# Kernel optimization log

Hardware: AMD Instinct MI355X
Metric: run time of the kernel (lower is better)

The kernel has to match this reference:

```python
import jax, jax.numpy as jnp
import numpy as np

# dims
L, H, ENC, DM, DFF, S, P, B = 2, 8, 862, 512, 2048, 512, 96, 32
HD = DM // H  # per-head q/k/v dim (v_dim = d_model, double_v_dim=False)


def setup_inputs() -> dict:
    key = jax.random.key(0)
    ks = jax.random.split(key, 16)
    rn = lambda k, shape, scale: jax.random.normal(k, shape, jnp.float32) * scale
    return {
        "X": rn(ks[0], (B, S, ENC), 1.0),
        "batch_x_mark": rn(ks[1], (B, S, 4), 1.0),
        "dec_inp": rn(ks[2], (B, P, ENC), 1.0),
        "batch_y_mark": rn(ks[3], (B, P, 4), 1.0),
        # retention params (stacked over layers / heads), init ~ randn/fan_in as in source
        "wq": rn(ks[4], (L, H, ENC, HD), 1.0 / ENC),
        "wk": rn(ks[5], (L, H, ENC, HD), 1.0 / ENC),
        "wv": rn(ks[6], (L, H, ENC, HD), 1.0 / ENC),
        "wg": rn(ks[7], (L, ENC, DM), 1.0 / ENC),
        "wo_ret": rn(ks[8], (L, DM, ENC), 1.0 / ENC),
        "gn_w": jnp.ones((L, DM)), "gn_b": jnp.zeros((L, DM)),
        "ln1_w": jnp.ones((L, ENC)), "ln1_b": jnp.zeros((L, ENC)),
        "ln2_w": jnp.ones((L, ENC)), "ln2_b": jnp.zeros((L, ENC)),
        # SGLU params, init randn/hidden_size as in source
        "sglu_u": rn(ks[9], (L, ENC, DM), 1.0 / DM),
        "sglu_v": rn(ks[10], (L, ENC, DM), 1.0 / DM),
        "sglu_o": rn(ks[11], (L, DM, ENC), 1.0 / DM),
        # temporal projection MLP (Linear init scale)
        "tp_w1": rn(ks[12], (S, DFF), (1.0 / S) ** 0.5),
        "tp_b1": jnp.zeros((DFF,)),
        "tp_w2": rn(ks[13], (DFF, P), (1.0 / DFF) ** 0.5),
        "tp_b2": jnp.zeros((P,)),
    }


def _layernorm(x, w, b, eps=1e-5):
    m = x.mean(-1, keepdims=True)
    v = x.var(-1, keepdims=True)  # biased variance, matches torch LayerNorm
    return (x - m) * jax.lax.rsqrt(v + eps) * w + b


def _decay_mask(seq_len, n_heads):
    # RetNet per-head decays: gamma_h = 1 - exp(linspace(log 1/32, log 1/512, H))
    g = 1.0 - jnp.exp(jnp.linspace(jnp.log(1.0 / 32.0), jnp.log(1.0 / 512.0), n_heads))
    i = jnp.arange(seq_len)
    d = i[:, None] - i[None, :]
    return jnp.where(d >= 0, g[:, None, None] ** jnp.maximum(d, 0), 0.0)  # [H,S,S]


def _retention(x, wq, wk, wv, wg, wo, gnw, gnb, D):
    # x: [B,S,ENC]; wq/wk/wv: [H,ENC,HD]
    Q = jnp.einsum('bsi,hid->bhsd', x, wq)
    K = jnp.einsum('bsi,hid->bhsd', x, wk)
    V = jnp.einsum('bsi,hid->bhsd', x, wv)
    scores = jnp.einsum('bhsd,bhtd->bhst', Q, K) * D  # decay-masked retention
    Y = jnp.einsum('bhst,bhtv->bhsv', scores, V)      # [B,H,S,HD]
    # GroupNorm(groups=H) over concatenated head channels == per-head normalize
    m = Y.mean(-1, keepdims=True)
    v = Y.var(-1, keepdims=True)
    Yn = (Y - m) * jax.lax.rsqrt(v + 1e-5)
    Yn = Yn.transpose(0, 2, 1, 3).reshape(x.shape[0], x.shape[1], -1)  # [B,S,DM]
    Yn = Yn * gnw + gnb
    G = x @ wg
    return (G * jax.nn.sigmoid(G) * Yn) @ wo  # swish gate, project back to ENC


def reference(X, batch_x_mark, dec_inp, batch_y_mark, wq, wk, wv, wg, wo_ret,
              gn_w, gn_b, ln1_w, ln1_b, ln2_w, ln2_b, sglu_u, sglu_v, sglu_o,
              tp_w1, tp_b1, tp_w2, tp_b2):
    D = _decay_mask(X.shape[1], H)
    for i in range(L):
        Y = _retention(_layernorm(X, ln1_w[i], ln1_b[i]), wq[i], wk[i], wv[i],
                       wg[i], wo_ret[i], gn_w[i], gn_b[i], D) + X
        Z = _layernorm(Y, ln2_w[i], ln2_b[i])
        X = ((Z @ sglu_v[i]) * (Z @ sglu_u[i])) @ sglu_o[i] + Y  # SGLU + residual
    T = X.transpose(0, 2, 1)  # [B,ENC,S]
    T = jax.nn.gelu(T @ tp_w1 + tp_b1, approximate=False)
    T = T @ tp_w2 + tp_b2
    return T.transpose(0, 2, 1)  # [B,P,ENC]
```

## Files before the change

kernel.cpp:

```cpp
#include <hip/hip_runtime.h>
#include <cstddef>
#include <cstdint>

#define L_    2
#define H_    8
#define ENC_  862
#define DM_   512
#define DFF_  2048
#define S_    512
#define P_    96
#define B_    32
#define HD_   64
#define EPAD_ 896
#define KPE_  896
#define XLD_  864
#define M1_   (B_*S_)
#define M2_   (B_*EPAD_)

typedef unsigned short u16;
typedef unsigned int   u32;
typedef u16   u16x8 __attribute__((ext_vector_type(8)));
typedef short s16x8 __attribute__((ext_vector_type(8)));
typedef float f32x4 __attribute__((ext_vector_type(4)));

__device__ __forceinline__ float b2f(u16 v) { return __uint_as_float(((u32)v) << 16); }
__device__ __forceinline__ u16 f2b(float f) {
    u32 u = __float_as_uint(f);
    u = (u + 0x7FFF + ((u >> 16) & 1)) >> 16;
    return (u16)u;
}
__device__ __forceinline__ float gelu_exact(float x) {
    return 0.5f * x * (1.f + erff(x * 0.70710678118654752f));
}

typedef __attribute__((address_space(1))) const void gas_void;
typedef __attribute__((address_space(3))) void sas_void;
__device__ __forceinline__ void gload16(const u16* g, u16* l) {
    __builtin_amdgcn_global_load_lds((gas_void*)g, (sas_void*)l, 16, 0, 0);
}

__global__ __launch_bounds__(256) void zgap(u16* __restrict__ p, int n)
{
    int i = blockIdx.x * 256 + threadIdx.x;
    if (i < n) p[i] = 0;
}

template<int MODE, bool RF32>
__global__ __launch_bounds__(256) void mgemm(
    const u16* __restrict__ A, int ldA,
    const u16* __restrict__ BT, int ldBT,
    void* __restrict__ Cv, int ldc,
    const void* __restrict__ R, int ldR,
    int M, int N, int KP)
{
    __shared__ u16 As[128 * 64];
    __shared__ u16 Bs[128 * 64];
    int tid = threadIdx.x;
    int l = tid & 63, w = tid >> 6;
    int m0 = blockIdx.x * 128, n0 = blockIdx.y * 128;
    int wm = (w >> 1) * 64, wn = (w & 1) * 64;
    int fr = l & 15, kb = l >> 4;

    f32x4 acc[4][4];
    #pragma unroll
    for (int i = 0; i < 4; i++)
        #pragma unroll
        for (int j = 0; j < 4; j++)
            acc[i][j] = (f32x4){0.f, 0.f, 0.f, 0.f};

    int arow = tid >> 3, acol = (tid & 7) * 8;
    const u16* ga = A + (size_t)(m0 + arow) * ldA + acol;
    const u16* gb = BT + (size_t)(n0 + arow) * ldBT + acol;
    u16* lA = As + tid * 8;
    u16* lB = Bs + tid * 8;

    for (int kt = 0; kt < KP; kt += 64) {
        #pragma unroll
        for (int c = 0; c < 4; c++) {
            gload16(ga + (size_t)(c * 32) * ldA, lA + c * 2048);
            gload16(gb + (size_t)(c * 32) * ldBT, lB + c * 2048);
        }
        ga += 64; gb += 64;
        __syncthreads();
        #pragma unroll
        for (int ks = 0; ks < 2; ks++) {
            s16x8 af[4], bf[4];
            #pragma unroll
            for (int i = 0; i < 4; i++) {
                af[i] = *(const s16x8*)&As[(wm + i * 16 + fr) * 64 + ks * 32 + kb * 8];
                bf[i] = *(const s16x8*)&Bs[(wn + i * 16 + fr) * 64 + ks * 32 + kb * 8];
            }
            #pragma unroll
            for (int i = 0; i < 4; i++)
                #pragma unroll
                for (int j = 0; j < 4; j++)
                    acc[i][j] = __builtin_amdgcn_mfma_f32_16x16x32_bf16(af[i], bf[j], acc[i][j], 0, 0, 0);
        }
        __syncthreads();
    }

    u16*   Cb = (u16*)Cv;
    float* Cf = (float*)Cv;
    const float* Rf = (const float*)R;
    const u16*   Rb = (const u16*)R;
    #pragma unroll
    for (int i = 0; i < 4; i++) {
        int mrow = m0 + wm + i * 16 + (l >> 4) * 4;
        #pragma unroll
        for (int j = 0; j < 4; j++) {
            int ncol = n0 + wn + j * 16 + (l & 15);
            if (ncol >= N) continue;
            #pragma unroll
            for (int r = 0; r < 4; r++) {
                int m = mrow + r;
                float v = acc[i][j][r];
                if (MODE == 0) {
                    Cb[(size_t)m * ldc + ncol] = f2b(v);
                } else if (MODE == 1) {
                    v += RF32 ? Rf[(size_t)m * ldR + ncol] : b2f(Rb[(size_t)m * ldR + ncol]);
                    Cb[(size_t)m * ldc + ncol] = f2b(v);
                } else if (MODE == 2) {
                    Cb[(size_t)m * ldc + ncol] = f2b(gelu_exact(v + Rf[ncol]));
                } else {
                    int bb = m / EPAD_;
                    int e = m - bb * EPAD_;
                    if (e < ENC_)
                        Cf[((size_t)bb * P_ + ncol) * ENC_ + e] = v + Rf[ncol];
                }
            }
        }
    }
}

template<bool XF32>
__global__ __launch_bounds__(128) void ln_k(const void* __restrict__ xv, int ldin,
                                            const float* __restrict__ w,
                                            const float* __restrict__ b,
                                            u16* __restrict__ y)
{
    int row = blockIdx.x;
    const float* xf = (const float*)xv + (size_t)row * ldin;
    const u16*   xb = (const u16*)xv + (size_t)row * ldin;
    float s = 0.f, q = 0.f;
    for (int c = threadIdx.x; c < ENC_; c += 128) {
        float v = XF32 ? xf[c] : b2f(xb[c]);
        s += v; q += v * v;
    }
    #pragma unroll
    for (int m = 1; m < 64; m <<= 1) { s += __shfl_xor(s, m, 64); q += __shfl_xor(q, m, 64); }
    __shared__ float red[4];
    int wid = threadIdx.x >> 6;
    if ((threadIdx.x & 63) == 0) { red[wid] = s; red[2 + wid] = q; }
    __syncthreads();
    s = red[0] + red[1]; q = red[2] + red[3];
    float mean = s * (1.f / ENC_);
    float var = q * (1.f / ENC_) - mean * mean;
    float rs = rsqrtf(var + 1e-5f);
    u16* yr = y + (size_t)row * XLD_;
    for (int c = threadIdx.x; c < XLD_; c += 128) {
        u16 o = 0;
        if (c < ENC_) {
            float v = XF32 ? xf[c] : b2f(xb[c]);
            o = f2b((v - mean) * rs * w[c] + b[c]);
        }
        yr[c] = o;
    }
}

__global__ __launch_bounds__(256) void repackT(const float* __restrict__ src, u16* __restrict__ dst,
                                               int Nsrc, int Ksrc, int KP, int total)
{
    int idx = blockIdx.x * 256 + threadIdx.x;
    if (idx >= total) return;
    int n = idx / KP, k = idx - n * KP;
    dst[idx] = (k < Ksrc && n < Nsrc) ? f2b(src[(size_t)k * Nsrc + n]) : (u16)0;
}

__global__ __launch_bounds__(256) void repack_qkvg(const float* __restrict__ wq, const float* __restrict__ wk,
                                                   const float* __restrict__ wv, const float* __restrict__ wg,
                                                   u16* __restrict__ dst)
{
    int idx = blockIdx.x * 256 + threadIdx.x;
    if (idx >= 2048 * KPE_) return;
    int n = idx / KPE_, k = idx - n * KPE_;
    u16 v = 0;
    if (k < ENC_) {
        int sec = n >> 9, c = n & 511;
        if (sec == 3) v = f2b(wg[(size_t)k * DM_ + c]);
        else {
            const float* s = (sec == 0) ? wq : (sec == 1) ? wk : wv;
            int h = c >> 6, d = c & 63;
            v = f2b(s[((size_t)h * ENC_ + k) * HD_ + d]);
        }
    }
    dst[idx] = v;
}

__global__ __launch_bounds__(256) void gate1_k(const u16* __restrict__ QKVG,
                                               const u16* __restrict__ Yn,
                                               u16* __restrict__ out)
{
    int i = blockIdx.x * 256 + threadIdx.x;
    int row = i >> 6, col = (i & 63) * 8;
    u16x8 g = *(const u16x8*)&QKVG[(size_t)row * 2048 + 1536 + col];
    u16x8 yv = *(const u16x8*)&Yn[(size_t)row * 512 + col];
    u16x8 o;
    #pragma unroll
    for (int j = 0; j < 8; j++) {
        float gf = b2f(g[j]);
        o[j] = f2b(gf / (1.f + __expf(-gf)) * b2f(yv[j]));
    }
    *(u16x8*)&out[(size_t)row * 512 + col] = o;
}

__global__ __launch_bounds__(256) void gate2_k(const u16* __restrict__ Z, u16* __restrict__ out)
{
    int i = blockIdx.x * 256 + threadIdx.x;
    int row = i >> 6, col = (i & 63) * 8;
    u16x8 a = *(const u16x8*)&Z[(size_t)row * 1024 + col];
    u16x8 b = *(const u16x8*)&Z[(size_t)row * 1024 + 512 + col];
    u16x8 o;
    #pragma unroll
    for (int j = 0; j < 8; j++) o[j] = f2b(b2f(a[j]) * b2f(b[j]));
    *(u16x8*)&out[(size_t)row * 512 + col] = o;
}

__global__ __launch_bounds__(256) void transpose_k(const u16* __restrict__ Xf, u16* __restrict__ XT)
{
    __shared__ u16 t[64][65];
    int b = blockIdx.x, s0 = blockIdx.y * 64, e0 = blockIdx.z * 64;
    int tid = threadIdx.x;
    int sr = tid >> 2, ch = (tid & 3) * 16;
    const u16* src = Xf + ((size_t)(b * S_) + s0 + sr) * ENC_ + e0 + ch;
    #pragma unroll
    for (int i = 0; i < 16; i++)
        t[sr][ch + i] = (e0 + ch + i < ENC_) ? src[i] : (u16)0;
    __syncthreads();
    int er = tid >> 2;
    u16* dst = XT + ((size_t)b * EPAD_ + e0 + er) * 512 + s0 + ch;
    #pragma unroll
    for (int i = 0; i < 16; i++)
        dst[i] = t[ch + i][er];
}

__global__ __launch_bounds__(256) void retention_k(const u16* __restrict__ QKVG,
                                                   const float* __restrict__ gnw,
                                                   const float* __restrict__ gnb,
                                                   u16* __restrict__ Yn)
{
    __shared__ u16 Ks[64 * 72];
    __shared__ u16 Vt[64 * 72];
    __shared__ u16 Pl[64 * 72];
    int tid = threadIdx.x;
    int l = tid & 63, w = tid >> 6;
    int g = l >> 4, fr = l & 15;
    int st = blockIdx.x, bh = blockIdx.y;
    int b = bh >> 3, h = bh & 7;
    int s0 = st * 64;

    const float lo = -3.46573590280f;
    const float hi = -6.23832462504f;
    float gamma = 1.f - expf(lo + (float)h * ((hi - lo) * (1.f / 7.f)));
    float l2g = log2f(gamma);

    size_t qbase = (size_t)(b * S_) * 2048 + h * 64;

    int qs_rel = w * 16 + fr;
    float qscale = exp2f((float)qs_rel * l2g);
    s16x8 qa[2];
    {
        const u16* qsrc = QKVG + qbase + (size_t)(s0 + qs_rel) * 2048;
        #pragma unroll
        for (int ks = 0; ks < 2; ks++) {
            u16x8 raw = *(const u16x8*)(qsrc + ks * 32 + g * 8);
            s16x8 sc;
            #pragma unroll
            for (int e = 0; e < 8; e++) sc[e] = (short)f2b(b2f(raw[e]) * qscale);
            qa[ks] = sc;
        }
    }

    f32x4 accy[4];
    #pragma unroll
    for (int jj = 0; jj < 4; jj++) accy[jj] = (f32x4){0.f, 0.f, 0.f, 0.f};

    int tv = tid >> 2, dv0 = (tid & 3) * 16;

    for (int tt = 0; tt <= st; ++tt) {
        int t0 = tt * 64;
        __syncthreads();
        {
            float kscale = exp2f((float)(s0 - (t0 + tv)) * l2g);
            const u16* ksrc = QKVG + qbase + (size_t)(t0 + tv) * 2048 + 512 + dv0;
            const u16* vsrc = QKVG + qbase + (size_t)(t0 + tv) * 2048 + 1024 + dv0;
            u16x8 k0 = *(const u16x8*)ksrc;
            u16x8 k1 = *(const u16x8*)(ksrc + 8);
            s16x8 o0, o1;
            #pragma unroll
            for (int e = 0; e < 8; e++) {
                o0[e] = (short)f2b(b2f(k0[e]) * kscale);
                o1[e] = (short)f2b(b2f(k1[e]) * kscale);
            }
            *(s16x8*)&Ks[tv * 72 + dv0]     = o0;
            *(s16x8*)&Ks[tv * 72 + dv0 + 8] = o1;
            u16x8 v0 = *(const u16x8*)vsrc;
            u16x8 v1 = *(const u16x8*)(vsrc + 8);
            #pragma unroll
            for (int e = 0; e < 8; e++) {
                Vt[(dv0 + e) * 72 + tv]     = v0[e];
                Vt[(dv0 + 8 + e) * 72 + tv] = v1[e];
            }
        }
        __syncthreads();

        f32x4 ps[4];
        #pragma unroll
        for (int j = 0; j < 4; j++) ps[j] = (f32x4){0.f, 0.f, 0.f, 0.f};
        #pragma unroll
        for (int ks = 0; ks < 2; ks++) {
            #pragma unroll
            for (int j = 0; j < 4; j++) {
                s16x8 kf = *(const s16x8*)&Ks[(j * 16 + fr) * 72 + ks * 32 + g * 8];
                ps[j] = __builtin_amdgcn_mfma_f32_16x16x32_bf16(qa[ks], kf, ps[j], 0, 0, 0);
            }
        }
        bool diag = (tt == st);
        #pragma unroll
        for (int j = 0; j < 4; j++) {
            #pragma unroll
            for (int r = 0; r < 4; r++) {
                int srel = w * 16 + g * 4 + r;
                int tloc = j * 16 + fr;
                float p = ps[j][r];
                if (diag && (srel < tloc)) p = 0.f;
                Pl[srel * 72 + tloc] = f2b(p);
            }
        }
        s16x8 pa0 = *(const s16x8*)&Pl[(w * 16 + fr) * 72 + g * 8];
        s16x8 pa1 = *(const s16x8*)&Pl[(w * 16 + fr) * 72 + 32 + g * 8];
        #pragma unroll
        for (int jj = 0; jj < 4; jj++) {
            s16x8 vb0 = *(const s16x8*)&Vt[(jj * 16 + fr) * 72 + g * 8];
            s16x8 vb1 = *(const s16x8*)&Vt[(jj * 16 + fr) * 72 + 32 + g * 8];
            accy[jj] = __builtin_amdgcn_mfma_f32_16x16x32_bf16(pa0, vb0, accy[jj], 0, 0, 0);
            accy[jj] = __builtin_amdgcn_mfma_f32_16x16x32_bf16(pa1, vb1, accy[jj], 0, 0, 0);
        }
    }

    #pragma unroll
    for (int r = 0; r < 4; r++) {
        float s_ = accy[0][r] + accy[1][r] + accy[2][r] + accy[3][r];
        float q_ = accy[0][r]*accy[0][r] + accy[1][r]*accy[1][r]
                 + accy[2][r]*accy[2][r] + accy[3][r]*accy[3][r];
        #pragma unroll
        for (int m = 1; m < 16; m <<= 1) { s_ += __shfl_xor(s_, m, 64); q_ += __shfl_xor(q_, m, 64); }
        float mean = s_ * (1.f / 64.f);
        float var = q_ * (1.f / 64.f) - mean * mean;
        float rs = rsqrtf(var + 1e-5f);
        int srow = s0 + w * 16 + g * 4 + r;
        #pragma unroll
        for (int jj = 0; jj < 4; jj++) {
            int c0 = h * 64 + jj * 16 + fr;
            Yn[(size_t)(b * S_ + srow) * 512 + c0] =
                f2b((accy[jj][r] - mean) * rs * gnw[c0] + gnb[c0]);
        }
    }
}

extern "C" void kernel_launch(void* const* d_in, const int* in_sizes, int n_in,
                              void* d_out, int out_size, void* d_ws, size_t ws_size,
                              hipStream_t stream)
{
    const float* X    = (const float*)d_in[0];
    const float* wq   = (const float*)d_in[4];
    const float* wk   = (const float*)d_in[5];
    const float* wv   = (const float*)d_in[6];
    const float* wg   = (const float*)d_in[7];
    const float* wo   = (const float*)d_in[8];
    const float* gnw  = (const float*)d_in[9];
    const float* gnb  = (const float*)d_in[10];
    const float* ln1w = (const float*)d_in[11];
    const float* ln1b = (const float*)d_in[12];
    const float* ln2w = (const float*)d_in[13];
    const float* ln2b = (const float*)d_in[14];
    const float* su   = (const float*)d_in[15];
    const float* sv   = (const float*)d_in[16];
    const float* so   = (const float*)d_in[17];
    const float* tw1  = (const float*)d_in[18];
    const float* tb1  = (const float*)d_in[19];
    const float* tw2  = (const float*)d_in[20];
    const float* tb2  = (const float*)d_in[21];
    u16* ws = (u16*)d_ws;

    const size_t NXE = (size_t)M1_ * ENC_;
    const size_t oA  = 0;
    const size_t oB  = (size_t)M1_ * XLD_ + 1024;
    const size_t oC  = oB + (size_t)M1_ * 2048;
    const size_t oD  = oC + (size_t)M1_ * 512;
    const size_t oE  = oD + (size_t)M1_ * 512;
    const size_t oF  = oE + NXE;
    const size_t oW  = oF + NXE;
    const size_t oWqkvg = oW;
    const size_t oWo    = oWqkvg + (size_t)2048 * KPE_;
    const size_t oWsuv  = oWo + (size_t)EPAD_ * 512;
    const size_t oWso   = oWsuv + (size_t)1024 * KPE_;
    const size_t oWt1   = oWso + (size_t)EPAD_ * 512;
    const size_t oWt2   = oWt1 + (size_t)2048 * 512;
    const size_t END    = oWt2 + (size_t)128 * 2048;
    const size_t oXT = 0;
    const size_t oT1 = (size_t)B_ * EPAD_ * 512;
    if (ws_size < END * sizeof(u16)) return;

    u16* bufXn = ws + oA;
    u16* bufQKVG = ws + oB;
    u16* bufZ = ws + oB;
    u16* bufYn = ws + oC;
    u16* bufGD = ws + oD;
    u16* bufY = ws + oE;
    u16* bufF = ws + oF;
    u16* wqkvgT = ws + oWqkvg;
    u16* woT = ws + oWo;
    u16* suvT = ws + oWsuv;
    u16* soT = ws + oWso;
    u16* tw1T = ws + oWt1;
    u16* tw2T = ws + oWt2;
    u16* XT = ws + oXT;
    u16* T1 = ws + oT1;

    dim3 blk(256);
    const size_t NW = (size_t)ENC_ * DM_;

    zgap<<<dim3(4), blk, 0, stream>>>(ws + (size_t)M1_ * XLD_, 1024);

    for (int l = 0; l < L_; ++l) {
        repack_qkvg<<<dim3((2048 * KPE_ + 255) / 256), blk, 0, stream>>>(
            wq + l * NW, wk + l * NW, wv + l * NW, wg + l * NW, wqkvgT);
        repackT<<<dim3((EPAD_ * 512 + 255) / 256), blk, 0, stream>>>(wo + l * NW, woT, ENC_, DM_, 512, EPAD_ * 512);
        repackT<<<dim3((512 * KPE_ + 255) / 256), blk, 0, stream>>>(su + l * NW, suvT, DM_, ENC_, KPE_, 512 * KPE_);
        repackT<<<dim3((512 * KPE_ + 255) / 256), blk, 0, stream>>>(sv + l * NW, suvT + (size_t)512 * KPE_, DM_, ENC_, KPE_, 512 * KPE_);
        repackT<<<dim3((EPAD_ * 512 + 255) / 256), blk, 0, stream>>>(so + l * NW, soT, ENC_, DM_, 512, EPAD_ * 512);

        if (l == 0)
            ln_k<true ><<<dim3(M1_), dim3(128), 0, stream>>>(X,    ENC_, ln1w + l * ENC_, ln1b + l * ENC_, bufXn);
        else
            ln_k<false><<<dim3(M1_), dim3(128), 0, stream>>>(bufF, ENC_, ln1w + l * ENC_, ln1b + l * ENC_, bufXn);

        mgemm<0, false><<<dim3(M1_ / 128, 16), blk, 0, stream>>>(bufXn, XLD_, wqkvgT, KPE_,
                                                                 bufQKVG, 2048, nullptr, 0, M1_, 2048, KPE_);

        retention_k<<<dim3(S_ / 64, B_ * H_), blk, 0, stream>>>(bufQKVG, gnw + l * DM_, gnb + l * DM_, bufYn);

        gate1_k<<<dim3(M1_ * 64 / 256), blk, 0, stream>>>(bufQKVG, bufYn, bufGD);

        if (l == 0)
            mgemm<1, true ><<<dim3(M1_ / 128, 7), blk, 0, stream>>>(bufGD, 512, woT, 512,
                                                                    bufY, ENC_, X, ENC_, M1_, ENC_, 512);
        else
            mgemm<1, false><<<dim3(M1_ / 128, 7), blk, 0, stream>>>(bufGD, 512, woT, 512,
                                                                    bufY, ENC_, bufF, ENC_, M1_, ENC_, 512);

        ln_k<false><<<dim3(M1_), dim3(128), 0, stream>>>(bufY, ENC_, ln2w + l * ENC_, ln2b + l * ENC_, bufXn);

        mgemm<0, false><<<dim3(M1_ / 128, 8), blk, 0, stream>>>(bufXn, XLD_, suvT, KPE_,
                                                                bufZ, 1024, nullptr, 0, M1_, 1024, KPE_);

        gate2_k<<<dim3(M1_ * 64 / 256), blk, 0, stream>>>(bufZ, bufGD);

        mgemm<1, false><<<dim3(M1_ / 128, 7), blk, 0, stream>>>(bufGD, 512, soT, 512,
                                                                bufF, ENC_, bufY, ENC_, M1_, ENC_, 512);
    }

    repackT<<<dim3((2048 * 512 + 255) / 256), blk, 0, stream>>>(tw1, tw1T, DFF_, S_, 512, 2048 * 512);
    repackT<<<dim3((128 * 2048 + 255) / 256), blk, 0, stream>>>(tw2, tw2T, P_, DFF_, 2048, 128 * 2048);

    transpose_k<<<dim3(B_, S_ / 64, EPAD_ / 64), blk, 0, stream>>>(bufF, XT);

    mgemm<2, false><<<dim3(M2_ / 128, 16), blk, 0, stream>>>(XT, 512, tw1T, 512,
                                                             T1, DFF_, tb1, 0, M2_, DFF_, 512);
    mgemm<3, false><<<dim3(M2_ / 128, 1), blk, 0, stream>>>(T1, DFF_, tw2T, 2048,
                                                            d_out, 0, tb2, 0, M2_, P_, 2048);
}
```

Measured before the change: 1.174 ms.

## Double-buffer GEMM LDS tiles and fuse swish gate into retention epilogue

The bf16 MFMA GEMM now keeps two LDS buffers for its A and B tiles. The global-to-LDS load of the next K tile is issued before the MFMAs on the current tile, so memory latency can overlap with compute. The separate gate1 kernel is removed: the retention kernel's GroupNorm epilogue reads the gate column, applies the swish, and writes the gated output directly, saving one launch and a round trip of the Yn buffer. In exchange the GEMM's LDS footprint doubles to 64KB per block, which can lower the number of resident blocks per CU.

```diff
diff --git a/kernel.cpp b/kernel.cpp
--- a/kernel.cpp
+++ b/kernel.cpp
@@ -53,8 +53,8 @@
     const void* __restrict__ R, int ldR,
     int M, int N, int KP)
 {
-    __shared__ u16 As[128 * 64];
-    __shared__ u16 Bs[128 * 64];
+    __shared__ u16 As[2][128 * 64];
+    __shared__ u16 Bs[2][128 * 64];
     int tid = threadIdx.x;
     int l = tid & 63, w = tid >> 6;
     int m0 = blockIdx.x * 128, n0 = blockIdx.y * 128;
@@ -69,26 +69,34 @@
             acc[i][j] = (f32x4){0.f, 0.f, 0.f, 0.f};
 
     int arow = tid >> 3, acol = (tid & 7) * 8;
-    const u16* ga = A + (size_t)(m0 + arow) * ldA + acol;
-    const u16* gb = BT + (size_t)(n0 + arow) * ldBT + acol;
-    u16* lA = As + tid * 8;
-    u16* lB = Bs + tid * 8;
-
-    for (int kt = 0; kt < KP; kt += 64) {
+    const u16* gaBase = A + (size_t)(m0 + arow) * ldA + acol;
+    const u16* gbBase = BT + (size_t)(n0 + arow) * ldBT + acol;
+
+    auto stage = [&](int kofs, int bufi) {
+        const u16* ga = gaBase + kofs;
+        const u16* gb = gbBase + kofs;
+        u16* lA = As[bufi] + tid * 8;
+        u16* lB = Bs[bufi] + tid * 8;
         #pragma unroll
         for (int c = 0; c < 4; c++) {
             gload16(ga + (size_t)(c * 32) * ldA, lA + c * 2048);
             gload16(gb + (size_t)(c * 32) * ldBT, lB + c * 2048);
         }
-        ga += 64; gb += 64;
-        __syncthreads();
+    };
+
+    stage(0, 0);
+    __syncthreads();
+    int nt = KP >> 6;
+    for (int t = 0; t < nt; ++t) {
+        int cur = t & 1;
+        if (t + 1 < nt) stage((t + 1) << 6, cur ^ 1);
         #pragma unroll
         for (int ks = 0; ks < 2; ks++) {
             s16x8 af[4], bf[4];
             #pragma unroll
             for (int i = 0; i < 4; i++) {
-                af[i] = *(const s16x8*)&As[(wm + i * 16 + fr) * 64 + ks * 32 + kb * 8];
-                bf[i] = *(const s16x8*)&Bs[(wn + i * 16 + fr) * 64 + ks * 32 + kb * 8];
+                af[i] = *(const s16x8*)&As[cur][(wm + i * 16 + fr) * 64 + ks * 32 + kb * 8];
+                bf[i] = *(const s16x8*)&Bs[cur][(wn + i * 16 + fr) * 64 + ks * 32 + kb * 8];
             }
             #pragma unroll
             for (int i = 0; i < 4; i++)
@@ -196,23 +204,6 @@
     dst[idx] = v;
 }
 
-__global__ __launch_bounds__(256) void gate1_k(const u16* __restrict__ QKVG,
-                                               const u16* __restrict__ Yn,
-                                               u16* __restrict__ out)
-{
-    int i = blockIdx.x * 256 + threadIdx.x;
-    int row = i >> 6, col = (i & 63) * 8;
-    u16x8 g = *(const u16x8*)&QKVG[(size_t)row * 2048 + 1536 + col];
-    u16x8 yv = *(const u16x8*)&Yn[(size_t)row * 512 + col];
-    u16x8 o;
-    #pragma unroll
-    for (int j = 0; j < 8; j++) {
-        float gf = b2f(g[j]);
-        o[j] = f2b(gf / (1.f + __expf(-gf)) * b2f(yv[j]));
-    }
-    *(u16x8*)&out[(size_t)row * 512 + col] = o;
-}
-
 __global__ __launch_bounds__(256) void gate2_k(const u16* __restrict__ Z, u16* __restrict__ out)
 {
     int i = blockIdx.x * 256 + threadIdx.x;
@@ -246,7 +237,7 @@
 __global__ __launch_bounds__(256) void retention_k(const u16* __restrict__ QKVG,
                                                    const float* __restrict__ gnw,
                                                    const float* __restrict__ gnb,
-                                                   u16* __restrict__ Yn)
+                                                   u16* __restrict__ GD)
 {
     __shared__ u16 Ks[64 * 72];
     __shared__ u16 Vt[64 * 72];
@@ -361,8 +352,10 @@
         #pragma unroll
         for (int jj = 0; jj < 4; jj++) {
             int c0 = h * 64 + jj * 16 + fr;
-            Yn[(size_t)(b * S_ + srow) * 512 + c0] =
-                f2b((accy[jj][r] - mean) * rs * gnw[c0] + gnb[c0]);
+            float yn = (accy[jj][r] - mean) * rs * gnw[c0] + gnb[c0];
+            float gf = b2f(QKVG[(size_t)(b * S_ + srow) * 2048 + 1536 + c0]);
+            GD[(size_t)(b * S_ + srow) * 512 + c0] =
+                f2b(gf / (1.f + __expf(-gf)) * yn);
         }
     }
 }
@@ -414,7 +407,6 @@
     u16* bufXn = ws + oA;
     u16* bufQKVG = ws + oB;
     u16* bufZ = ws + oB;
-    u16* bufYn = ws + oC;
     u16* bufGD = ws + oD;
     u16* bufY = ws + oE;
     u16* bufF = ws + oF;
@@ -448,9 +440,7 @@
         mgemm<0, false><<<dim3(M1_ / 128, 16), blk, 0, stream>>>(bufXn, XLD_, wqkvgT, KPE_,
                                                                  bufQKVG, 2048, nullptr, 0, M1_, 2048, KPE_);
 
-        retention_k<<<dim3(S_ / 64, B_ * H_), blk, 0, stream>>>(bufQKVG, gnw + l * DM_, gnb + l * DM_, bufYn);
-
-        gate1_k<<<dim3(M1_ * 64 / 256), blk, 0, stream>>>(bufQKVG, bufYn, bufGD);
+        retention_k<<<dim3(S_ / 64, B_ * H_), blk, 0, stream>>>(bufQKVG, gnw + l * DM_, gnb + l * DM_, bufGD);
 
         if (l == 0)
             mgemm<1, true ><<<dim3(M1_ / 128, 7), blk, 0, stream>>>(bufGD, 512, woT, 512,
```

Result: no change. 1.168 ms (-0.5%).
